# Kernel tuning notes

Measured on AMD Instinct MI355X. Metric: run time of the kernel, lower is better.

## Reference

```python
import jax, jax.numpy as jnp
import numpy as np

# Dimensions
B, C, H, W = 16, 256, 32, 32
CO, DK, DV, NH = 256, 128, 128, 8   # channels_out, depth_k, depth_v, num_heads
KS = 3                              # conv kernel size
DKH, DVH = DK // NH, DV // NH


def setup_inputs() -> dict:
    key = jax.random.key(0)
    ks = jax.random.split(key, 4)
    s = 0.05
    return {
        "x": jax.random.normal(ks[0], (B, C, H, W), jnp.float32),
        # conv branch: 3x3 conv -> channels_out - depth_v = 128, HWIO layout
        "conv_w": jax.random.normal(ks[1], (KS, KS, C, CO - DV), jnp.float32) * s,
        "conv_b": jnp.zeros((CO - DV,), jnp.float32),
        # 1x1 QKV conv: 2*depth_k + depth_v output channels
        "qkv_w": jax.random.normal(ks[2], (2 * DK + DV, C), jnp.float32) * s,
        "qkv_b": jnp.zeros((2 * DK + DV,), jnp.float32),
        # 1x1 output projection conv: depth_v -> depth_v
        "proj_w": jax.random.normal(ks[3], (DV, DV), jnp.float32) * s,
        "proj_b": jnp.zeros((DV,), jnp.float32),
    }


def reference(x, conv_w, conv_b, qkv_w, qkv_b, proj_w, proj_b):
    # --- conv branch (3x3, SAME padding, NCHW) ---
    conv_out = jax.lax.conv_general_dilated(
        x, conv_w, window_strides=(1, 1), padding='SAME',
        dimension_numbers=('NCHW', 'HWIO', 'NCHW'))
    conv_out = conv_out + conv_b[None, :, None, None]

    # --- attention branch ---
    # 1x1 conv == channel matmul
    kqv = jnp.einsum('bchw,oc->bohw', x, qkv_w) + qkv_b[None, :, None, None]
    # tf.split order: k, q, v
    k, q, v = jnp.split(kqv, [DK, 2 * DK], axis=1)
    q = q * (DKH ** -0.5)

    def heads(t, d):  # (B, NH*d, H, W) -> (B, NH, H*W, d)
        return t.reshape(B, NH, d, H * W).transpose(0, 1, 3, 2)

    qh, kh, vh = heads(q, DKH), heads(k, DKH), heads(v, DVH)
    logits = jnp.einsum('bnqd,bnkd->bnqk', qh, kh)          # (B,NH,HW,HW)
    weights = jax.nn.softmax(logits, axis=-1)
    attn = jnp.einsum('bnqk,bnkd->bnqd', weights, vh)       # (B,NH,HW,DVH)
    # combine heads, head-major channel order -> (B, DV, H, W)
    attn = attn.transpose(0, 1, 3, 2).reshape(B, DV, H, W)
    attn_out = jnp.einsum('bchw,oc->bohw', attn, proj_w) + proj_b[None, :, None, None]

    return jnp.concatenate([conv_out, attn_out], axis=1)
```

## Files before the change

### kernel.cpp

```cpp
#include <hip/hip_runtime.h>
#include <hip/hip_bf16.h>


#define Bn   16
#define Cin  256
#define HWp  1024
#define COn  256
#define NHn  8

typedef short short8  __attribute__((ext_vector_type(8)));
typedef short short4v __attribute__((ext_vector_type(4)));
typedef float f32x4   __attribute__((ext_vector_type(4)));
typedef float f32x16  __attribute__((ext_vector_type(16)));

__device__ inline short bf16_rne(float f) {
  unsigned u = __builtin_bit_cast(unsigned, f);
  u += 0x7fffu + ((u >> 16) & 1u);
  return (short)(u >> 16);
}

__device__ inline unsigned pkbf(float a, float b) {
  __hip_bfloat162 h = __float22bfloat162_rn(make_float2(a, b));
  unsigned u;
  __builtin_memcpy(&u, &h, 4);
  return u;
}

__device__ inline void store_bf8(short* dst, const float* f) {
  uint4 u;
  u.x = pkbf(f[0], f[1]); u.y = pkbf(f[2], f[3]);
  u.z = pkbf(f[4], f[5]); u.w = pkbf(f[6], f[7]);
  *(uint4*)dst = u;
}

__global__ __launch_bounds__(256) void prep_fused(
    const float* __restrict__ cw, const float* __restrict__ qw,
    const float* __restrict__ pw, const float* __restrict__ x,
    short* __restrict__ wfc, short* __restrict__ wfq,
    short* __restrict__ wfp, short* __restrict__ xt)
{
  __shared__ short t[32][262];
  const int tid = threadIdx.x;
  if (blockIdx.x < 200) {
    const int gid  = blockIdx.x * 256 + tid;
    const int lane = gid & 63, frag = gid >> 6;
    const int l15 = lane & 15, q = lane >> 4;
    short8 pk;
    if (frag < 576) {
      const int cf = frag & 7, cq = (frag >> 3) & 7, kk = frag >> 6;
      const int co = cf * 16 + l15, c = cq * 32 + q * 8;
#pragma unroll
      for (int j = 0; j < 8; ++j)
        pk[j] = bf16_rne(cw[(size_t)(kk * Cin + c + j) * 128 + co]);
      *(short8*)(wfc + (size_t)frag * 512 + lane * 8) = pk;
    } else if (frag < 768) {
      const int f = frag - 576;
      const int rt = f >> 3, kf = f & 7;
      const int o = rt * 16 + l15, c = kf * 32 + q * 8;
#pragma unroll
      for (int j = 0; j < 8; ++j) pk[j] = bf16_rne(qw[o * Cin + c + j]);
      *(short8*)(wfq + (size_t)f * 512 + lane * 8) = pk;
    } else if (frag < 800) {
      const int f = frag - 768;
      const int rt = f >> 2, kf = f & 3;
      const int o = rt * 16 + l15, c = kf * 32 + q * 8;
#pragma unroll
      for (int j = 0; j < 8; ++j) pk[j] = bf16_rne(pw[o * 128 + c + j]);
      *(short8*)(wfp + (size_t)f * 512 + lane * 8) = pk;
    }
  } else {
    const int bid = blockIdx.x - 200;
    const int hw0 = (bid & 3) * 256;
    const int c0  = ((bid >> 2) & 7) * 32;
    const int b   = bid >> 5;
#pragma unroll 4
    for (int cc = 0; cc < 32; ++cc)
      t[cc][tid] = bf16_rne(x[(size_t)(b * Cin + c0 + cc) * HWp + hw0 + tid]);
    __syncthreads();
    for (int s = tid; s < 1024; s += 256) {
      const int hwl = s >> 2, q4 = s & 3;
      short8 pk;
#pragma unroll
      for (int j = 0; j < 8; ++j) pk[j] = t[q4 * 8 + j][hwl];
      *(short8*)&xt[((size_t)(b * HWp + hw0 + hwl)) * 256 + c0 + q4 * 8] = pk;
    }
  }
}

__global__ __launch_bounds__(256) void conv_mfma(
    const short* __restrict__ xt, const short* __restrict__ wf,
    const float* __restrict__ bias, float* __restrict__ out)
{
  __shared__ short xl[2][102 * 42];
  const int tid  = threadIdx.x;
  const int lane = tid & 63, wv = tid >> 6;
  const int l15  = lane & 15, g = lane >> 4;
  const int b  = blockIdx.x >> 5;
  const int h0 = blockIdx.x & 31;

  f32x4 acc[2][2] = {};
  short8 rv[2];

#define LOADC(c0_)                                                            \
  {                                                                           \
    _Pragma("unroll")                                                         \
    for (int i = 0; i < 2; ++i) {                                             \
      const int s = tid + i * 256;                                            \
      if (s < 408) {                                                          \
        const int cell = s >> 2, qq = s & 3;                                  \
        const int r = cell / 34, col = cell - r * 34;                         \
        const int h_in = h0 - 1 + r, w_in = col - 1;                          \
        short8 v = {};                                                        \
        if (h_in >= 0 && h_in < 32 && w_in >= 0 && w_in < 32)                 \
          v = *(const short8*)&xt[((size_t)(b * HWp + h_in * 32 + w_in)) * 256\
                                  + (c0_) + qq * 8];                          \
        rv[i] = v;                                                            \
      }                                                                       \
    }                                                                         \
  }
#define WRITEC(bi_)                                                           \
  {                                                                           \
    _Pragma("unroll")                                                         \
    for (int i = 0; i < 2; ++i) {                                             \
      const int s = tid + i * 256;                                            \
      if (s < 408) {                                                          \
        const int cell = s >> 2, qq = s & 3;                                  \
        *(short8*)&xl[bi_][cell * 42 + qq * 8] = rv[i];                       \
      }                                                                       \
    }                                                                         \
  }

  LOADC(0); WRITEC(0);
  __syncthreads();

  for (int cq = 0; cq < 8; ++cq) {
    if (cq < 7) LOADC((cq + 1) * 32);
    const short* cur = xl[cq & 1];
#pragma unroll
    for (int kk = 0; kk < 9; ++kk) {
      const int kh = kk / 3, kw = kk - kh * 3;
#pragma unroll
      for (int af = 0; af < 2; ++af) {
        const short8 a0 = *(const short8*)(wf + (size_t)((kk * 8 + cq) * 8 + wv * 2 + af) * 512 + lane * 8);
#pragma unroll
        for (int bf = 0; bf < 2; ++bf) {
          const int m = bf * 16 + l15;
          const short8 xv = *(const short8*)&cur[(kh * 34 + m + kw) * 42 + g * 8];
          acc[af][bf] = __builtin_amdgcn_mfma_f32_16x16x32_bf16(a0, xv, acc[af][bf], 0, 0, 0);
        }
      }
    }
    if (cq < 7) WRITEC((cq + 1) & 1);
    __syncthreads();
  }
#undef LOADC
#undef WRITEC

#pragma unroll
  for (int af = 0; af < 2; ++af)
#pragma unroll
    for (int r = 0; r < 4; ++r) {
      const int co = (wv * 2 + af) * 16 + 4 * g + r;
      const float bv = bias[co];
      float* op = out + (size_t)(b * COn + co) * HWp + h0 * 32 + l15;
      op[0]  = acc[af][0][r] + bv;
      op[16] = acc[af][1][r] + bv;
    }
}

__global__ __launch_bounds__(512) void qkv_mfma(
    const short* __restrict__ xt, const short* __restrict__ wfq,
    const float* __restrict__ bias, short* __restrict__ qbuf,
    short* __restrict__ kbuf, short* __restrict__ vtbuf)
{
  __shared__ short xl[16384];
  const int tid = threadIdx.x, lane = tid & 63, wv = tid >> 6;
  const int l15 = lane & 15, g = lane >> 4;
  const int hw0 = blockIdx.x * 64;
  const int b   = blockIdx.y;

  {
    const int qq = tid & 3, kf = (tid >> 2) & 7, hl = tid >> 5;
#pragma unroll
    for (int mt = 0; mt < 4; ++mt) {
      const int p  = ((mt * 8 + kf) * 4 + qq) * 16 + hl;
      const int sw = p ^ ((p >> 4) & 7);
      const short8 v = *(const short8*)&xt[((size_t)(b * HWp + hw0 + mt * 16 + hl)) * 256
                                           + kf * 32 + qq * 8];
      *(short8*)&xl[sw * 8] = v;
    }
  }
  __syncthreads();

  f32x4 acc[3][4] = {};
  for (int kf = 0; kf < 8; ++kf) {
    short8 bfr[4];
#pragma unroll
    for (int mt = 0; mt < 4; ++mt) {
      const int q  = ((mt * 8 + kf) * 4 + g) * 16 + l15;
      const int sw = q ^ ((q >> 4) & 7);
      bfr[mt] = *(const short8*)&xl[sw * 8];
    }
#pragma unroll
    for (int i = 0; i < 3; ++i) {
      const int rt = wv * 3 + i;
      const short8 af = *(const short8*)(wfq + ((size_t)(rt * 8 + kf) * 64 + lane) * 8);
#pragma unroll
      for (int mt = 0; mt < 4; ++mt)
        acc[i][mt] = __builtin_amdgcn_mfma_f32_16x16x32_bf16(af, bfr[mt], acc[i][mt], 0, 0, 0);
    }
  }

#pragma unroll
  for (int i = 0; i < 3; ++i) {
    const int rt = wv * 3 + i;
    float bv[4];
#pragma unroll
    for (int r = 0; r < 4; ++r) bv[r] = bias[rt * 16 + 4 * g + r];
    if (rt < 8) {
      short* kp = kbuf + ((size_t)(b * NHn + rt) * HWp + hw0) * 16 + 4 * g;
#pragma unroll
      for (int mt = 0; mt < 4; ++mt) {
        short4v s;
#pragma unroll
        for (int r = 0; r < 4; ++r) s[r] = bf16_rne(acc[i][mt][r] + bv[r]);
        *(short4v*)(kp + (size_t)(mt * 16 + l15) * 16) = s;
      }
    } else if (rt < 16) {
      short* qp = qbuf + ((size_t)(b * NHn + rt - 8) * HWp + hw0) * 16 + 4 * g;
#pragma unroll
      for (int mt = 0; mt < 4; ++mt) {
        short4v s;
#pragma unroll
        for (int r = 0; r < 4; ++r) s[r] = bf16_rne((acc[i][mt][r] + bv[r]) * 0.25f);
        *(short4v*)(qp + (size_t)(mt * 16 + l15) * 16) = s;
      }
    } else {
      short* vp = vtbuf + (size_t)(b * NHn + rt - 16) * 16 * HWp;
#pragma unroll
      for (int mt = 0; mt < 4; ++mt)
#pragma unroll
        for (int r = 0; r < 4; ++r)
          vp[(size_t)(4 * g + r) * HWp + hw0 + mt * 16 + l15] =
              bf16_rne(acc[i][mt][r] + bv[r]);
    }
  }
}

__global__ __launch_bounds__(256) void attn_mfma(
    const short* __restrict__ qb, const short* __restrict__ kb,
    const short* __restrict__ vt, float* __restrict__ abuf)
{
  __shared__ short P[4][2][32][40];
  const int tid = threadIdx.x, lane = tid & 63, wv = tid >> 6;
  const int l15 = lane & 15, g = lane >> 4;
  const int l31 = lane & 31, hi = lane >> 5;
  const int h = blockIdx.y, b = blockIdx.z, bh = b * NHn + h;
  const int q0 = blockIdx.x * 128 + wv * 32;

  const short* qp = qb + (size_t)bh * HWp * 16;
  const short* kp = kb + (size_t)bh * HWp * 16;
  const short* vp = vt + (size_t)bh * 16 * HWp;

  const short8 qf = *(const short8*)(qp + (size_t)(q0 + l31) * 16 + hi * 8);

  f32x4 o0 = {}, o1 = {};
  float lsum = 0.f;

  for (int kt = 0; kt < HWp; kt += 64) {
#pragma unroll
    for (int t = 0; t < 2; ++t) {
      const int k0 = kt + t * 32;
      const short8 kf = *(const short8*)(kp + (size_t)(k0 + l31) * 16 + hi * 8);
      f32x16 z = {};
      const f32x16 s = __builtin_amdgcn_mfma_f32_32x32x16_bf16(kf, qf, z, 0, 0, 0);
      float p[16];
#pragma unroll
      for (int r = 0; r < 16; ++r) { p[r] = __expf(s[r]); lsum += p[r]; }
#pragma unroll
      for (int rg = 0; rg < 4; ++rg) {
        uint2 u;
        u.x = pkbf(p[4 * rg + 0], p[4 * rg + 1]);
        u.y = pkbf(p[4 * rg + 2], p[4 * rg + 3]);
        *(uint2*)&P[wv][t][l31][8 * rg + 4 * hi] = u;
      }
      const short8 vf = *(const short8*)(vp + (size_t)l15 * HWp + k0 + g * 8);
      const short8 pf0 = *(const short8*)&P[wv][t][l15][g * 8];
      o0 = __builtin_amdgcn_mfma_f32_16x16x32_bf16(vf, pf0, o0, 0, 0, 0);
      const short8 pf1 = *(const short8*)&P[wv][t][16 + l15][g * 8];
      o1 = __builtin_amdgcn_mfma_f32_16x16x32_bf16(vf, pf1, o1, 0, 0, 0);
    }
  }

  const float l  = lsum + __shfl_xor(lsum, 32);
  const float li0 = 1.f / __shfl(l, l15);
  const float li1 = 1.f / __shfl(l, 16 + l15);
#pragma unroll
  for (int r = 0; r < 4; ++r) {
    const int d = 4 * g + r;
    float* op = abuf + (size_t)(b * 128 + h * 16 + d) * HWp + q0;
    op[l15]      = o0[r] * li0;
    op[16 + l15] = o1[r] * li1;
  }
}

__global__ __launch_bounds__(256) void proj_mfma(
    const float* __restrict__ a, const short* __restrict__ wfp,
    const float* __restrict__ bias, float* __restrict__ out)
{
  __shared__ short xl[8192];
  const int tid = threadIdx.x, lane = tid & 63, wv = tid >> 6;
  const int l15 = lane & 15, g = lane >> 4;
  const int hw0 = blockIdx.x * 64;
  const int b   = blockIdx.y;

#pragma unroll
  for (int it = 0; it < 4; ++it) {
    const int p  = it * 256 + tid;
    const int mt = p >> 8, kf = (p >> 6) & 3, qq = (p >> 4) & 3, hl = p & 15;
    const float* ap = a + (size_t)(b * 128 + kf * 32 + qq * 8) * HWp
                        + hw0 + mt * 16 + hl;
    float fv[8];
#pragma unroll
    for (int j = 0; j < 8; ++j) fv[j] = ap[(size_t)j * HWp];
    store_bf8(&xl[p * 8], fv);
  }
  __syncthreads();

  f32x4 acc[2][4] = {};
  for (int kf = 0; kf < 4; ++kf) {
    short8 bfr[4];
#pragma unroll
    for (int mt = 0; mt < 4; ++mt)
      bfr[mt] = *(const short8*)&xl[(((mt * 4 + kf) * 4 + g) * 16 + l15) * 8];
#pragma unroll
    for (int i = 0; i < 2; ++i) {
      const int rt = wv * 2 + i;
      const short8 af = *(const short8*)(wfp + ((size_t)(rt * 4 + kf) * 64 + lane) * 8);
#pragma unroll
      for (int mt = 0; mt < 4; ++mt)
        acc[i][mt] = __builtin_amdgcn_mfma_f32_16x16x32_bf16(af, bfr[mt], acc[i][mt], 0, 0, 0);
    }
  }

#pragma unroll
  for (int i = 0; i < 2; ++i) {
    const int rt = wv * 2 + i;
#pragma unroll
    for (int r = 0; r < 4; ++r) {
      const int o = rt * 16 + 4 * g + r;
      const float bv = bias[o];
      float* op = out + (size_t)(b * COn + 128 + o) * HWp + hw0 + l15;
#pragma unroll
      for (int mt = 0; mt < 4; ++mt)
        op[mt * 16] = acc[i][mt][r] + bv;
    }
  }
}

extern "C" void kernel_launch(void* const* d_in, const int* in_sizes, int n_in,
                              void* d_out, int out_size, void* d_ws, size_t ws_size,
                              hipStream_t stream) {
  const float* x      = (const float*)d_in[0];
  const float* conv_w = (const float*)d_in[1];
  const float* conv_b = (const float*)d_in[2];
  const float* qkv_w  = (const float*)d_in[3];
  const float* qkv_b  = (const float*)d_in[4];
  const float* proj_w = (const float*)d_in[5];
  const float* proj_b = (const float*)d_in[6];
  float* out = (float*)d_out;

  char* wsb = (char*)d_ws;
  short* wfc    = (short*)wsb;
  short* wfq    = (short*)(wsb + (1u << 20));
  short* wfp    = (short*)(wsb + (2u << 20));
  short* qbuf16 = (short*)(wsb + (8u << 20));
  short* kbuf16 = (short*)(wsb + (12u << 20));
  short* vtbuf  = (short*)(wsb + (16u << 20));
  float* abuf   = (float*)(wsb + (20u << 20));
  short* xtbuf  = (short*)(wsb + (28u << 20));

  prep_fused<<<dim3(712), 256, 0, stream>>>(conv_w, qkv_w, proj_w, x,
                                            wfc, wfq, wfp, xtbuf);
  conv_mfma <<<dim3(512), 256, 0, stream>>>(xtbuf, wfc, conv_b, out);
  qkv_mfma  <<<dim3(16, 16), 512, 0, stream>>>(xtbuf, wfq, qkv_b, qbuf16, kbuf16, vtbuf);
  attn_mfma <<<dim3(8, 8, 16), 256, 0, stream>>>(qbuf16, kbuf16, vtbuf, abuf);
  proj_mfma <<<dim3(16, 16), 256, 0, stream>>>(abuf, wfp, proj_b, out);
}
```

Baseline: 169.9 us.

## Fuse conv and QKV into one launch, emit attention output as bf16 HW-major

Merges the 3x3 conv kernel and the QKV 1x1 kernel into a single launch whose blocks alternate between conv rows and QKV tiles. This removes one launch and lets both independent GEMMs run concurrently on the GPU. The conv path now preloads all 18 weight fragments per channel chunk into registers, and QKV blocks shrink to 32 pixels with 256 threads. The attention kernel writes its output as packed bf16 in [b, hw, channel] layout, so the projection can load it with contiguous vector reads instead of strided fp32 gathers, which also halves that buffer's traffic. Costs include higher register pressure in the fused kernel and divergent block roles sharing one LDS allocation.

```diff
diff --git a/kernel.cpp b/kernel.cpp
--- a/kernel.cpp
+++ b/kernel.cpp
@@ -24,13 +24,6 @@
   unsigned u;
   __builtin_memcpy(&u, &h, 4);
   return u;
-}
-
-__device__ inline void store_bf8(short* dst, const float* f) {
-  uint4 u;
-  u.x = pkbf(f[0], f[1]); u.y = pkbf(f[2], f[3]);
-  u.z = pkbf(f[4], f[5]); u.w = pkbf(f[6], f[7]);
-  *(uint4*)dst = u;
 }
 
 __global__ __launch_bounds__(256) void prep_fused(
@@ -87,169 +80,169 @@
   }
 }
 
-__global__ __launch_bounds__(256) void conv_mfma(
-    const short* __restrict__ xt, const short* __restrict__ wf,
-    const float* __restrict__ bias, float* __restrict__ out)
+__global__ __launch_bounds__(256) void convqkv_fused(
+    const short* __restrict__ xt, const short* __restrict__ wfc,
+    const short* __restrict__ wfq, const float* __restrict__ cbias,
+    const float* __restrict__ qbias, float* __restrict__ out,
+    short* __restrict__ qbuf, short* __restrict__ kbuf,
+    short* __restrict__ vtbuf)
 {
-  __shared__ short xl[2][102 * 42];
-  const int tid  = threadIdx.x;
-  const int lane = tid & 63, wv = tid >> 6;
-  const int l15  = lane & 15, g = lane >> 4;
-  const int b  = blockIdx.x >> 5;
-  const int h0 = blockIdx.x & 31;
-
-  f32x4 acc[2][2] = {};
-  short8 rv[2];
+  __shared__ short lds[2 * 102 * 42];
+  const int tid = threadIdx.x, lane = tid & 63, wv = tid >> 6;
+  const int l15 = lane & 15, g = lane >> 4;
+  const int part = blockIdx.x & 1, idx = blockIdx.x >> 1;
+  const int b = idx >> 5;
+
+  if (part == 0) {
+    const int h0 = idx & 31;
+    f32x4 acc[2][2] = {};
+    short8 rv[2];
+    short8 acur[9][2];
 
 #define LOADC(c0_)                                                            \
-  {                                                                           \
-    _Pragma("unroll")                                                         \
-    for (int i = 0; i < 2; ++i) {                                             \
-      const int s = tid + i * 256;                                            \
-      if (s < 408) {                                                          \
-        const int cell = s >> 2, qq = s & 3;                                  \
-        const int r = cell / 34, col = cell - r * 34;                         \
-        const int h_in = h0 - 1 + r, w_in = col - 1;                          \
-        short8 v = {};                                                        \
-        if (h_in >= 0 && h_in < 32 && w_in >= 0 && w_in < 32)                 \
-          v = *(const short8*)&xt[((size_t)(b * HWp + h_in * 32 + w_in)) * 256\
-                                  + (c0_) + qq * 8];                          \
-        rv[i] = v;                                                            \
+    {                                                                         \
+      _Pragma("unroll")                                                       \
+      for (int i = 0; i < 2; ++i) {                                           \
+        const int s = tid + i * 256;                                          \
+        if (s < 408) {                                                        \
+          const int cell = s >> 2, qq = s & 3;                                \
+          const int r = cell / 34, col = cell - r * 34;                       \
+          const int h_in = h0 - 1 + r, w_in = col - 1;                        \
+          short8 v = {};                                                      \
+          if (h_in >= 0 && h_in < 32 && w_in >= 0 && w_in < 32)               \
+            v = *(const short8*)&xt[((size_t)(b * HWp + h_in * 32 + w_in))    \
+                                    * 256 + (c0_) + qq * 8];                  \
+          rv[i] = v;                                                          \
+        }                                                                     \
       }                                                                       \
-    }                                                                         \
-  }
+    }
 #define WRITEC(bi_)                                                           \
-  {                                                                           \
-    _Pragma("unroll")                                                         \
-    for (int i = 0; i < 2; ++i) {                                             \
-      const int s = tid + i * 256;                                            \
-      if (s < 408) {                                                          \
-        const int cell = s >> 2, qq = s & 3;                                  \
-        *(short8*)&xl[bi_][cell * 42 + qq * 8] = rv[i];                       \
+    {                                                                         \
+      _Pragma("unroll")                                                       \
+      for (int i = 0; i < 2; ++i) {                                           \
+        const int s = tid + i * 256;                                          \
+        if (s < 408) {                                                        \
+          const int cell = s >> 2, qq = s & 3;                                \
+          *(short8*)&lds[(bi_) * 4284 + cell * 42 + qq * 8] = rv[i];          \
+        }                                                                     \
       }                                                                       \
-    }                                                                         \
-  }
-
-  LOADC(0); WRITEC(0);
-  __syncthreads();
-
-  for (int cq = 0; cq < 8; ++cq) {
-    if (cq < 7) LOADC((cq + 1) * 32);
-    const short* cur = xl[cq & 1];
-#pragma unroll
-    for (int kk = 0; kk < 9; ++kk) {
-      const int kh = kk / 3, kw = kk - kh * 3;
-#pragma unroll
-      for (int af = 0; af < 2; ++af) {
-        const short8 a0 = *(const short8*)(wf + (size_t)((kk * 8 + cq) * 8 + wv * 2 + af) * 512 + lane * 8);
-#pragma unroll
-        for (int bf = 0; bf < 2; ++bf) {
-          const int m = bf * 16 + l15;
-          const short8 xv = *(const short8*)&cur[(kh * 34 + m + kw) * 42 + g * 8];
-          acc[af][bf] = __builtin_amdgcn_mfma_f32_16x16x32_bf16(a0, xv, acc[af][bf], 0, 0, 0);
-        }
-      }
-    }
-    if (cq < 7) WRITEC((cq + 1) & 1);
+    }
+
+    LOADC(0); WRITEC(0);
     __syncthreads();
-  }
+
+    for (int cq = 0; cq < 8; ++cq) {
+#pragma unroll
+      for (int kk = 0; kk < 9; ++kk)
+#pragma unroll
+        for (int af = 0; af < 2; ++af)
+          acur[kk][af] = *(const short8*)(wfc +
+              (size_t)((kk * 8 + cq) * 8 + wv * 2 + af) * 512 + lane * 8);
+      if (cq < 7) LOADC((cq + 1) * 32);
+      const short* cur = lds + (cq & 1) * 4284;
+#pragma unroll
+      for (int kk = 0; kk < 9; ++kk) {
+        const int kh = kk / 3, kw = kk - kh * 3;
+        short8 xv[2];
+#pragma unroll
+        for (int bf = 0; bf < 2; ++bf)
+          xv[bf] = *(const short8*)&cur[(kh * 34 + bf * 16 + l15 + kw) * 42 + g * 8];
+#pragma unroll
+        for (int af = 0; af < 2; ++af)
+#pragma unroll
+          for (int bf = 0; bf < 2; ++bf)
+            acc[af][bf] = __builtin_amdgcn_mfma_f32_16x16x32_bf16(
+                acur[kk][af], xv[bf], acc[af][bf], 0, 0, 0);
+      }
+      if (cq < 7) WRITEC((cq + 1) & 1);
+      __syncthreads();
+    }
 #undef LOADC
 #undef WRITEC
 
 #pragma unroll
-  for (int af = 0; af < 2; ++af)
-#pragma unroll
-    for (int r = 0; r < 4; ++r) {
-      const int co = (wv * 2 + af) * 16 + 4 * g + r;
-      const float bv = bias[co];
-      float* op = out + (size_t)(b * COn + co) * HWp + h0 * 32 + l15;
-      op[0]  = acc[af][0][r] + bv;
-      op[16] = acc[af][1][r] + bv;
-    }
-}
-
-__global__ __launch_bounds__(512) void qkv_mfma(
-    const short* __restrict__ xt, const short* __restrict__ wfq,
-    const float* __restrict__ bias, short* __restrict__ qbuf,
-    short* __restrict__ kbuf, short* __restrict__ vtbuf)
-{
-  __shared__ short xl[16384];
-  const int tid = threadIdx.x, lane = tid & 63, wv = tid >> 6;
-  const int l15 = lane & 15, g = lane >> 4;
-  const int hw0 = blockIdx.x * 64;
-  const int b   = blockIdx.y;
-
-  {
-    const int qq = tid & 3, kf = (tid >> 2) & 7, hl = tid >> 5;
-#pragma unroll
-    for (int mt = 0; mt < 4; ++mt) {
-      const int p  = ((mt * 8 + kf) * 4 + qq) * 16 + hl;
+    for (int af = 0; af < 2; ++af)
+#pragma unroll
+      for (int r = 0; r < 4; ++r) {
+        const int co = (wv * 2 + af) * 16 + 4 * g + r;
+        const float bv = cbias[co];
+        float* op = out + (size_t)(b * COn + co) * HWp + h0 * 32 + l15;
+        op[0]  = acc[af][0][r] + bv;
+        op[16] = acc[af][1][r] + bv;
+      }
+  } else {
+    const int hw0 = (idx & 31) * 32;
+
+#pragma unroll
+    for (int it = 0; it < 4; ++it) {
+      const int p  = it * 256 + tid;
+      const int hl = p & 15, qq = (p >> 4) & 3, kf = (p >> 6) & 7, mt = p >> 9;
+      const short8 v = *(const short8*)&xt[((size_t)(b * HWp + hw0 + mt * 16 + hl))
+                                           * 256 + kf * 32 + qq * 8];
       const int sw = p ^ ((p >> 4) & 7);
-      const short8 v = *(const short8*)&xt[((size_t)(b * HWp + hw0 + mt * 16 + hl)) * 256
-                                           + kf * 32 + qq * 8];
-      *(short8*)&xl[sw * 8] = v;
-    }
-  }
-  __syncthreads();
-
-  f32x4 acc[3][4] = {};
-  for (int kf = 0; kf < 8; ++kf) {
-    short8 bfr[4];
-#pragma unroll
-    for (int mt = 0; mt < 4; ++mt) {
-      const int q  = ((mt * 8 + kf) * 4 + g) * 16 + l15;
-      const int sw = q ^ ((q >> 4) & 7);
-      bfr[mt] = *(const short8*)&xl[sw * 8];
-    }
-#pragma unroll
-    for (int i = 0; i < 3; ++i) {
-      const int rt = wv * 3 + i;
-      const short8 af = *(const short8*)(wfq + ((size_t)(rt * 8 + kf) * 64 + lane) * 8);
-#pragma unroll
-      for (int mt = 0; mt < 4; ++mt)
-        acc[i][mt] = __builtin_amdgcn_mfma_f32_16x16x32_bf16(af, bfr[mt], acc[i][mt], 0, 0, 0);
-    }
-  }
-
-#pragma unroll
-  for (int i = 0; i < 3; ++i) {
-    const int rt = wv * 3 + i;
-    float bv[4];
-#pragma unroll
-    for (int r = 0; r < 4; ++r) bv[r] = bias[rt * 16 + 4 * g + r];
-    if (rt < 8) {
-      short* kp = kbuf + ((size_t)(b * NHn + rt) * HWp + hw0) * 16 + 4 * g;
-#pragma unroll
-      for (int mt = 0; mt < 4; ++mt) {
-        short4v s;
-#pragma unroll
-        for (int r = 0; r < 4; ++r) s[r] = bf16_rne(acc[i][mt][r] + bv[r]);
-        *(short4v*)(kp + (size_t)(mt * 16 + l15) * 16) = s;
-      }
-    } else if (rt < 16) {
-      short* qp = qbuf + ((size_t)(b * NHn + rt - 8) * HWp + hw0) * 16 + 4 * g;
-#pragma unroll
-      for (int mt = 0; mt < 4; ++mt) {
-        short4v s;
-#pragma unroll
-        for (int r = 0; r < 4; ++r) s[r] = bf16_rne((acc[i][mt][r] + bv[r]) * 0.25f);
-        *(short4v*)(qp + (size_t)(mt * 16 + l15) * 16) = s;
-      }
-    } else {
-      short* vp = vtbuf + (size_t)(b * NHn + rt - 16) * 16 * HWp;
-#pragma unroll
-      for (int mt = 0; mt < 4; ++mt)
-#pragma unroll
-        for (int r = 0; r < 4; ++r)
-          vp[(size_t)(4 * g + r) * HWp + hw0 + mt * 16 + l15] =
-              bf16_rne(acc[i][mt][r] + bv[r]);
+      *(short8*)&lds[sw * 8] = v;
+    }
+    __syncthreads();
+
+    f32x4 acc[6][2] = {};
+    for (int kf = 0; kf < 8; ++kf) {
+      short8 bfr[2];
+#pragma unroll
+      for (int mt = 0; mt < 2; ++mt) {
+        const int q  = ((mt * 8 + kf) * 4 + g) * 16 + l15;
+        const int sw = q ^ ((q >> 4) & 7);
+        bfr[mt] = *(const short8*)&lds[sw * 8];
+      }
+#pragma unroll
+      for (int i = 0; i < 6; ++i) {
+        const int rt = wv * 6 + i;
+        const short8 af = *(const short8*)(wfq + ((size_t)(rt * 8 + kf) * 64 + lane) * 8);
+#pragma unroll
+        for (int mt = 0; mt < 2; ++mt)
+          acc[i][mt] = __builtin_amdgcn_mfma_f32_16x16x32_bf16(af, bfr[mt], acc[i][mt], 0, 0, 0);
+      }
+    }
+
+#pragma unroll
+    for (int i = 0; i < 6; ++i) {
+      const int rt = wv * 6 + i;
+      float bv[4];
+#pragma unroll
+      for (int r = 0; r < 4; ++r) bv[r] = qbias[rt * 16 + 4 * g + r];
+      if (rt < 8) {
+        short* kp = kbuf + ((size_t)(b * NHn + rt) * HWp + hw0) * 16 + 4 * g;
+#pragma unroll
+        for (int mt = 0; mt < 2; ++mt) {
+          short4v s;
+#pragma unroll
+          for (int r = 0; r < 4; ++r) s[r] = bf16_rne(acc[i][mt][r] + bv[r]);
+          *(short4v*)(kp + (size_t)(mt * 16 + l15) * 16) = s;
+        }
+      } else if (rt < 16) {
+        short* qp = qbuf + ((size_t)(b * NHn + rt - 8) * HWp + hw0) * 16 + 4 * g;
+#pragma unroll
+        for (int mt = 0; mt < 2; ++mt) {
+          short4v s;
+#pragma unroll
+          for (int r = 0; r < 4; ++r) s[r] = bf16_rne((acc[i][mt][r] + bv[r]) * 0.25f);
+          *(short4v*)(qp + (size_t)(mt * 16 + l15) * 16) = s;
+        }
+      } else {
+        short* vp = vtbuf + (size_t)(b * NHn + rt - 16) * 16 * HWp;
+#pragma unroll
+        for (int mt = 0; mt < 2; ++mt)
+#pragma unroll
+          for (int r = 0; r < 4; ++r)
+            vp[(size_t)(4 * g + r) * HWp + hw0 + mt * 16 + l15] =
+                bf16_rne(acc[i][mt][r] + bv[r]);
+      }
     }
   }
 }
 
 __global__ __launch_bounds__(256) void attn_mfma(
     const short* __restrict__ qb, const short* __restrict__ kb,
-    const short* __restrict__ vt, float* __restrict__ abuf)
+    const short* __restrict__ vt, short* __restrict__ at)
 {
   __shared__ short P[4][2][32][40];
   const int tid = threadIdx.x, lane = tid & 63, wv = tid >> 6;
@@ -295,17 +288,17 @@
   const float l  = lsum + __shfl_xor(lsum, 32);
   const float li0 = 1.f / __shfl(l, l15);
   const float li1 = 1.f / __shfl(l, 16 + l15);
-#pragma unroll
-  for (int r = 0; r < 4; ++r) {
-    const int d = 4 * g + r;
-    float* op = abuf + (size_t)(b * 128 + h * 16 + d) * HWp + q0;
-    op[l15]      = o0[r] * li0;
-    op[16 + l15] = o1[r] * li1;
-  }
+  uint2 u0, u1;
+  u0.x = pkbf(o0[0] * li0, o0[1] * li0);
+  u0.y = pkbf(o0[2] * li0, o0[3] * li0);
+  u1.x = pkbf(o1[0] * li1, o1[1] * li1);
+  u1.y = pkbf(o1[2] * li1, o1[3] * li1);
+  *(uint2*)&at[(size_t)(b * HWp + q0 + l15) * 128 + h * 16 + 4 * g]      = u0;
+  *(uint2*)&at[(size_t)(b * HWp + q0 + 16 + l15) * 128 + h * 16 + 4 * g] = u1;
 }
 
 __global__ __launch_bounds__(256) void proj_mfma(
-    const float* __restrict__ a, const short* __restrict__ wfp,
+    const short* __restrict__ at, const short* __restrict__ wfp,
     const float* __restrict__ bias, float* __restrict__ out)
 {
   __shared__ short xl[8192];
@@ -317,13 +310,11 @@
 #pragma unroll
   for (int it = 0; it < 4; ++it) {
     const int p  = it * 256 + tid;
-    const int mt = p >> 8, kf = (p >> 6) & 3, qq = (p >> 4) & 3, hl = p & 15;
-    const float* ap = a + (size_t)(b * 128 + kf * 32 + qq * 8) * HWp
-                        + hw0 + mt * 16 + hl;
-    float fv[8];
-#pragma unroll
-    for (int j = 0; j < 8; ++j) fv[j] = ap[(size_t)j * HWp];
-    store_bf8(&xl[p * 8], fv);
+    const int hl = p & 15, qq = (p >> 4) & 3, kf = (p >> 6) & 3, mt = p >> 8;
+    const short8 v = *(const short8*)&at[((size_t)(b * HWp + hw0 + mt * 16 + hl))
+                                         * 128 + kf * 32 + qq * 8];
+    const int sw = p ^ ((p >> 4) & 7);
+    *(short8*)&xl[sw * 8] = v;
   }
   __syncthreads();
 
@@ -331,8 +322,11 @@
   for (int kf = 0; kf < 4; ++kf) {
     short8 bfr[4];
 #pragma unroll
-    for (int mt = 0; mt < 4; ++mt)
-      bfr[mt] = *(const short8*)&xl[(((mt * 4 + kf) * 4 + g) * 16 + l15) * 8];
+    for (int mt = 0; mt < 4; ++mt) {
+      const int q  = ((mt * 4 + kf) * 4 + g) * 16 + l15;
+      const int sw = q ^ ((q >> 4) & 7);
+      bfr[mt] = *(const short8*)&xl[sw * 8];
+    }
 #pragma unroll
     for (int i = 0; i < 2; ++i) {
       const int rt = wv * 2 + i;
@@ -377,13 +371,13 @@
   short* qbuf16 = (short*)(wsb + (8u << 20));
   short* kbuf16 = (short*)(wsb + (12u << 20));
   short* vtbuf  = (short*)(wsb + (16u << 20));
-  float* abuf   = (float*)(wsb + (20u << 20));
+  short* atbuf  = (short*)(wsb + (20u << 20));
   short* xtbuf  = (short*)(wsb + (28u << 20));
 
-  prep_fused<<<dim3(712), 256, 0, stream>>>(conv_w, qkv_w, proj_w, x,
-                                            wfc, wfq, wfp, xtbuf);
-  conv_mfma <<<dim3(512), 256, 0, stream>>>(xtbuf, wfc, conv_b, out);
-  qkv_mfma  <<<dim3(16, 16), 512, 0, stream>>>(xtbuf, wfq, qkv_b, qbuf16, kbuf16, vtbuf);
-  attn_mfma <<<dim3(8, 8, 16), 256, 0, stream>>>(qbuf16, kbuf16, vtbuf, abuf);
-  proj_mfma <<<dim3(16, 16), 256, 0, stream>>>(abuf, wfp, proj_b, out);
-}
+  prep_fused   <<<dim3(712), 256, 0, stream>>>(conv_w, qkv_w, proj_w, x,
+                                               wfc, wfq, wfp, xtbuf);
+  convqkv_fused<<<dim3(1024), 256, 0, stream>>>(xtbuf, wfc, wfq, conv_b, qkv_b,
+                                                out, qbuf16, kbuf16, vtbuf);
+  attn_mfma    <<<dim3(8, 8, 16), 256, 0, stream>>>(qbuf16, kbuf16, vtbuf, atbuf);
+  proj_mfma    <<<dim3(16, 16), 256, 0, stream>>>(atbuf, wfp, proj_b, out);
+}
```

After: 204.5 us. 20.4% more time.
